# Kernel tuning notes

Hardware: AMD Instinct MI355X
Metric: run time of the kernel (lower is better)

The kernel has to match this reference:

```python
import jax, jax.numpy as jnp
import numpy as np

NUM_HEADS = 12


def setup_inputs() -> dict:
    key = jax.random.key(0)
    k1, k2, k3, k4, k5 = jax.random.split(key, 5)
    B, H, W, C = 8, 32, 32, 768
    x = jax.random.normal(k1, (B, H, W, C), dtype=jnp.float32)
    # torch nn.Linear weights: (out_features, in_features)
    qkv_w = jax.random.normal(k2, (3 * C, C), dtype=jnp.float32) * (C ** -0.5)
    qkv_b = jax.random.normal(k3, (3 * C,), dtype=jnp.float32) * 0.02
    proj_w = jax.random.normal(k4, (C, C), dtype=jnp.float32) * (C ** -0.5)
    proj_b = jax.random.normal(k5, (C,), dtype=jnp.float32) * 0.02
    return {"x": x, "qkv_w": qkv_w, "qkv_b": qkv_b, "proj_w": proj_w, "proj_b": proj_b}


def reference(x, qkv_w, qkv_b, proj_w, proj_b):
    B, H, W, C = x.shape
    nh = NUM_HEADS
    hd = C // nh
    scale = hd ** -0.5
    L = H * W
    # qkv projection: (B, L, 3C)
    qkv = jnp.einsum('bhwc,oc->bhwo', x, qkv_w) + qkv_b
    # -> (3, B*nh, L, hd)
    qkv = qkv.reshape(B, L, 3, nh, hd).transpose(2, 0, 3, 1, 4).reshape(3, B * nh, L, hd)
    q, k, v = qkv[0], qkv[1], qkv[2]
    # attention scores (B*nh, L, L)
    attn = jnp.einsum('bqd,bkd->bqk', q * scale, k)
    attn = jax.nn.softmax(attn, axis=-1)
    out = jnp.einsum('bqk,bkd->bqd', attn, v)  # (B*nh, L, hd)
    out = out.reshape(B, nh, H, W, hd).transpose(0, 2, 3, 1, 4).reshape(B, H, W, C)
    out = jnp.einsum('bhwc,oc->bhwo', out, proj_w) + proj_b
    return out
```

## Files before the change

### kernel.cpp

```cpp
#include <hip/hip_runtime.h>


typedef __attribute__((ext_vector_type(8))) __bf16 bf16x8;
typedef __attribute__((ext_vector_type(4))) __bf16 bf16x4;
typedef __attribute__((ext_vector_type(4))) float f32x4;

#define GLL16(g, l) __builtin_amdgcn_global_load_lds( \
    (const __attribute__((address_space(1))) void*)(g), \
    (__attribute__((address_space(3))) void*)(l), 16, 0, 0)

static __device__ __forceinline__ f32x4 mfma16(bf16x8 a, bf16x8 b, f32x4 c) {
  return __builtin_amdgcn_mfma_f32_16x16x32_bf16(a, b, c, 0, 0, 0);
}

static __device__ __forceinline__ float exp2_hw(float x) {
  return __builtin_amdgcn_exp2f(x);
}

static __device__ __forceinline__ int swz64(int row, int col) {
  return (row * 64 + col) ^ ((row & 7) << 3);
}

__global__ __launch_bounds__(256) void cvt_all(const float* __restrict__ x,
                                               const float* __restrict__ wq,
                                               const float* __restrict__ wp,
                                               __bf16* __restrict__ dst,
                                               int nx4, int nwq4, int total4) {
  const int i = blockIdx.x * 256 + threadIdx.x;
  if (i >= total4) return;
  const float* src;
  int off;
  if (i < nx4) { src = x; off = i; }
  else if (i < nx4 + nwq4) { src = wq; off = i - nx4; }
  else { src = wp; off = i - nx4 - nwq4; }
  const float4 v = *(const float4*)&src[(size_t)off * 4];
  bf16x4 o;
  o[0] = (__bf16)v.x; o[1] = (__bf16)v.y; o[2] = (__bf16)v.z; o[3] = (__bf16)v.w;
  *(bf16x4*)&dst[(size_t)i * 4] = o;
}

template <int EPI>
__global__ __launch_bounds__(256, 4) void gemm_nt(const __bf16* __restrict__ A,
                                                  const __bf16* __restrict__ Bw,
                                                  const float* __restrict__ bias,
                                                  float* __restrict__ out,
                                                  __bf16* __restrict__ Qb,
                                                  __bf16* __restrict__ Kb,
                                                  __bf16* __restrict__ Vtb,
                                                  int M, int N, int K) {
  __shared__ alignas(16) __bf16 smem[17408];
  const int tid = threadIdx.x;
  const int lane = tid & 63;
  const int wave = tid >> 6;
  const int wr = wave >> 1, wc = wave & 1;
  const int l15 = lane & 15, lhi = lane >> 4;
  const int mbase = blockIdx.x * 128;
  const int nbase = blockIdx.y * 128;

  f32x4 acc[4][4];
#pragma unroll
  for (int m = 0; m < 4; ++m)
#pragma unroll
    for (int n = 0; n < 4; ++n) acc[m][n] = (f32x4){0.f, 0.f, 0.f, 0.f};

  const int e0 = wave * 512 + lane * 8;
  const int e1 = e0 + 2048;
  const int ar0 = mbase + (e0 >> 5), ac0 = e0 & 31;
  const int ar1 = mbase + (e1 >> 5), ac1 = e1 & 31;
  const int br0 = nbase + (e0 >> 5);
  const int br1 = nbase + (e1 >> 5);

  const int nkt = K >> 5;

#define STAGE(t, bf) do { \
    const int kb_ = (t) << 5; \
    GLL16(A + (size_t)ar0 * K + kb_ + ac0, &smem[(bf) * 4096 + e0]); \
    GLL16(A + (size_t)ar1 * K + kb_ + ac1, &smem[(bf) * 4096 + e1]); \
    GLL16(Bw + (size_t)br0 * K + kb_ + ac0, &smem[8192 + (bf) * 4096 + e0]); \
    GLL16(Bw + (size_t)br1 * K + kb_ + ac1, &smem[8192 + (bf) * 4096 + e1]); \
  } while (0)

  STAGE(0, 0);

  for (int kt = 0; kt < nkt; ++kt) {
    const int cur = kt & 1;
    asm volatile("s_waitcnt vmcnt(0)" ::: "memory");
    __builtin_amdgcn_s_barrier();
    asm volatile("" ::: "memory");
    if (kt + 1 < nkt) STAGE(kt + 1, cur ^ 1);

    const __bf16* bufA = &smem[cur * 4096];
    const __bf16* bufB = &smem[8192 + cur * 4096];
    bf16x8 a[4], b[4];
#pragma unroll
    for (int m = 0; m < 4; ++m)
      a[m] = *(const bf16x8*)&bufA[(wr * 64 + m * 16 + l15) * 32 + lhi * 8];
#pragma unroll
    for (int n = 0; n < 4; ++n)
      b[n] = *(const bf16x8*)&bufB[(wc * 64 + n * 16 + l15) * 32 + lhi * 8];
#pragma unroll
    for (int m = 0; m < 4; ++m)
#pragma unroll
      for (int n = 0; n < 4; ++n)
        acc[m][n] = mfma16(a[m], b[n], acc[m][n]);
  }
#undef STAGE

  if (EPI == 0 && nbase >= 1536) {
    __syncthreads();
    __bf16* ldsT = &smem[0];
#pragma unroll
    for (int n = 0; n < 4; ++n) {
      const int gl = wc * 64 + n * 16 + l15;
      const float bv = bias[nbase + gl];
#pragma unroll
      for (int m = 0; m < 4; ++m) {
        bf16x4 pk;
#pragma unroll
        for (int i = 0; i < 4; ++i) pk[i] = (__bf16)(acc[m][n][i] + bv);
        *(bf16x4*)&ldsT[gl * 136 + wr * 64 + m * 16 + lhi * 4] = pk;
      }
    }
    __syncthreads();
    const int r = tid >> 1;
    const int half = tid & 1;
    const int head = ((nbase - 1536) >> 6) + (r >> 6);
    const int d = r & 63;
    const int bb = mbase >> 10;
    const int lbase = mbase & 1023;
    __bf16* dst = Vtb + ((size_t)(bb * 12 + head) * 64 + d) * 1024 + lbase + half * 64;
    const __bf16* srcl = &ldsT[r * 136 + half * 64];
#pragma unroll
    for (int j = 0; j < 8; ++j)
      *(bf16x8*)&dst[j * 8] = *(const bf16x8*)&srcl[j * 8];
    return;
  }

#pragma unroll
  for (int n = 0; n < 4; ++n) {
    const int gcol = nbase + wc * 64 + n * 16 + l15;
    const float bv = bias[gcol];
    if (EPI == 1) {
#pragma unroll
      for (int m = 0; m < 4; ++m)
#pragma unroll
        for (int i = 0; i < 4; ++i) {
          const int grow = mbase + wr * 64 + m * 16 + lhi * 4 + i;
          out[(size_t)grow * N + gcol] = acc[m][n][i] + bv;
        }
    } else {
      const int three = gcol / 768;
      const int rem = gcol - three * 768;
      const int head = rem >> 6;
      const int d = rem & 63;
#pragma unroll
      for (int m = 0; m < 4; ++m)
#pragma unroll
        for (int i = 0; i < 4; ++i) {
          const int grow = mbase + wr * 64 + m * 16 + lhi * 4 + i;
          const int bb = grow >> 10;
          const int lrow = grow & 1023;
          const int bh = bb * 12 + head;
          const float v = acc[m][n][i] + bv;
          if (three == 0)
            Qb[((size_t)bh * 1024 + lrow) * 64 + d] = (__bf16)(v * 0.18033688f);
          else
            Kb[((size_t)bh * 1024 + lrow) * 64 + d] = (__bf16)v;
        }
    }
  }
}

__global__ __launch_bounds__(512, 6) void attn_fwd(const __bf16* __restrict__ Q,
                                                   const __bf16* __restrict__ Kg,
                                                   const __bf16* __restrict__ Vt,
                                                   __bf16* __restrict__ O) {
  __shared__ alignas(16) __bf16 lK[2][64 * 64];
  __shared__ alignas(16) __bf16 lV[2][64 * 64];
  __shared__ alignas(16) __bf16 lP[8][16 * 72];
  const int tid = threadIdx.x, lane = tid & 63, wave = tid >> 6;
  const int l15 = lane & 15, lhi = lane >> 4;
  const int bh = blockIdx.x, qt = blockIdx.y;
  const int b = bh / 12, head = bh % 12;

  bf16x8 q[2];
  {
    const int qrow = qt * 128 + wave * 16 + l15;
#pragma unroll
    for (int kk = 0; kk < 2; ++kk)
      q[kk] = *(const bf16x8*)&Q[((size_t)bh * 1024 + qrow) * 64 + kk * 32 + lhi * 8];
  }

  f32x4 o[4];
  float mrun = -3.0e38f, lrun = 0.f;
#pragma unroll
  for (int n = 0; n < 4; ++n) o[n] = (f32x4){0.f, 0.f, 0.f, 0.f};

  const int q0b = tid * 16;
  const int p0b = q0b ^ (((q0b >> 7) & 7) << 4);
  const int e0 = q0b >> 1;
  const int kofs0 = p0b >> 1;
  const int vofs0 = (p0b >> 7) * 1024 + ((p0b & 127) >> 1);

  const __bf16* kbase = Kg + (size_t)bh * 1024 * 64;
  const __bf16* vbase = Vt + (size_t)bh * 64 * 1024;

  GLL16(kbase + kofs0, &lK[0][e0]);
  GLL16(vbase + vofs0, &lV[0][e0]);
  __syncthreads();

  for (int kv = 0; kv < 16; ++kv) {
    const int cur = kv & 1;
    if (kv + 1 < 16) {
      GLL16(kbase + (kv + 1) * 4096 + kofs0, &lK[cur ^ 1][e0]);
      GLL16(vbase + (kv + 1) * 64 + vofs0, &lV[cur ^ 1][e0]);
    }

    f32x4 s[4];
#pragma unroll
    for (int km = 0; km < 4; ++km) {
      bf16x8 k0 = *(const bf16x8*)&lK[cur][swz64(km * 16 + l15, lhi * 8)];
      bf16x8 k1 = *(const bf16x8*)&lK[cur][swz64(km * 16 + l15, 32 + lhi * 8)];
      f32x4 z = (f32x4){0.f, 0.f, 0.f, 0.f};
      z = mfma16(k0, q[0], z);
      z = mfma16(k1, q[1], z);
      s[km] = z;
    }

    float lm = s[0][0];
#pragma unroll
    for (int km = 0; km < 4; ++km)
#pragma unroll
      for (int i = 0; i < 4; ++i) lm = fmaxf(lm, s[km][i]);

    if (!__all(lm - mrun <= 8.f)) {
      float r = lm;
      r = fmaxf(r, __shfl_xor(r, 16));
      r = fmaxf(r, __shfl_xor(r, 32));
      const float mnew = fmaxf(mrun, r);
      const float alpha = exp2_hw(mrun - mnew);
      mrun = mnew;
      lrun *= alpha;
      float am[4];
#pragma unroll
      for (int i = 0; i < 4; ++i) am[i] = __shfl(alpha, (lhi << 2) | i, 64);
#pragma unroll
      for (int n = 0; n < 4; ++n)
#pragma unroll
        for (int i = 0; i < 4; ++i) o[n][i] *= am[i];
    }

    {
      float ps = 0.f;
#pragma unroll
      for (int km = 0; km < 4; ++km) {
        bf16x4 pk;
#pragma unroll
        for (int i = 0; i < 4; ++i) {
          const float p = exp2_hw(s[km][i] - mrun);
          ps += p;
          pk[i] = (__bf16)p;
        }
        *(bf16x4*)&lP[wave][l15 * 72 + km * 16 + lhi * 4] = pk;
      }
      lrun += ps;
    }

    bf16x8 vf[4][2];
#pragma unroll
    for (int n = 0; n < 4; ++n)
#pragma unroll
      for (int kk = 0; kk < 2; ++kk)
        vf[n][kk] = *(const bf16x8*)&lV[cur][swz64(n * 16 + l15, kk * 32 + lhi * 8)];
    {
      bf16x8 p0 = *(const bf16x8*)&lP[wave][l15 * 72 + lhi * 8];
      bf16x8 p1 = *(const bf16x8*)&lP[wave][l15 * 72 + 32 + lhi * 8];
#pragma unroll
      for (int n = 0; n < 4; ++n) {
        o[n] = mfma16(p0, vf[n][0], o[n]);
        o[n] = mfma16(p1, vf[n][1], o[n]);
      }
    }
    __syncthreads();
  }

  float r = lrun;
  r += __shfl_xor(r, 16);
  r += __shfl_xor(r, 32);
  const float inv = 1.f / r;
  float im[4];
#pragma unroll
  for (int i = 0; i < 4; ++i) im[i] = __shfl(inv, (lhi << 2) | i, 64);
#pragma unroll
  for (int i = 0; i < 4; ++i) {
    const int lrow = qt * 128 + wave * 16 + lhi * 4 + i;
#pragma unroll
    for (int n = 0; n < 4; ++n) {
      const int col = head * 64 + n * 16 + l15;
      O[((size_t)b * 1024 + lrow) * 768 + col] = (__bf16)(o[n][i] * im[i]);
    }
  }
}

extern "C" void kernel_launch(void* const* d_in, const int* in_sizes, int n_in,
                              void* d_out, int out_size, void* d_ws, size_t ws_size,
                              hipStream_t stream) {
  const float* x = (const float*)d_in[0];
  const float* qkv_w = (const float*)d_in[1];
  const float* qkv_b = (const float*)d_in[2];
  const float* proj_w = (const float*)d_in[3];
  const float* proj_b = (const float*)d_in[4];
  float* out = (float*)d_out;

  const size_t NX = (size_t)8192 * 768;
  const size_t NWQ = (size_t)2304 * 768;
  const size_t NWP = (size_t)768 * 768;
  const size_t SZ = (size_t)96 * 1024 * 64;

  __bf16* xb = (__bf16*)d_ws;
  __bf16* wqkvb = xb + NX;
  __bf16* wprojb = wqkvb + NWQ;
  __bf16* Q = wprojb + NWP;
  __bf16* K = Q + SZ;
  __bf16* Vt = K + SZ;
  __bf16* AO = Vt + SZ;

  const int nx4 = (int)(NX / 4), nwq4 = (int)(NWQ / 4), nwp4 = (int)(NWP / 4);
  const int total4 = nx4 + nwq4 + nwp4;
  cvt_all<<<(total4 + 255) / 256, 256, 0, stream>>>(x, qkv_w, proj_w, xb, nx4, nwq4, total4);

  gemm_nt<0><<<dim3(64, 18), 256, 0, stream>>>(xb, wqkvb, qkv_b, nullptr, Q, K, Vt,
                                               8192, 2304, 768);
  attn_fwd<<<dim3(96, 8), 512, 0, stream>>>(Q, K, Vt, AO);
  gemm_nt<1><<<dim3(64, 6), 256, 0, stream>>>(AO, wprojb, proj_b, out,
                                              nullptr, nullptr, nullptr, 8192, 768, 768);
}
```

Baseline: 115.7 us.

## Double GEMM K-tile to 64 with XOR-swizzled LDS layout

The bf16 NT GEMM now stages K-tiles of 64 instead of 32. This halves the number of barrier/wait iterations and doubles the MFMA work per sync. The LDS layout is XOR-swizzled: global loads gather pre-swizzled source addresses so that the row-stride-64 fragment reads avoid bank conflicts. LDS use per block roughly doubles to 64KB, and launch bounds drop to 2 blocks per CU, which reduces occupancy.

```diff
diff --git a/kernel.cpp b/kernel.cpp
--- a/kernel.cpp
+++ b/kernel.cpp
@@ -19,6 +19,9 @@
 
 static __device__ __forceinline__ int swz64(int row, int col) {
   return (row * 64 + col) ^ ((row & 7) << 3);
+}
+static __device__ __forceinline__ int swz64e(int e) {
+  return e ^ (((e >> 6) & 7) << 3);
 }
 
 __global__ __launch_bounds__(256) void cvt_all(const float* __restrict__ x,
@@ -40,7 +43,7 @@
 }
 
 template <int EPI>
-__global__ __launch_bounds__(256, 4) void gemm_nt(const __bf16* __restrict__ A,
+__global__ __launch_bounds__(256, 2) void gemm_nt(const __bf16* __restrict__ A,
                                                   const __bf16* __restrict__ Bw,
                                                   const float* __restrict__ bias,
                                                   float* __restrict__ out,
@@ -48,7 +51,7 @@
                                                   __bf16* __restrict__ Kb,
                                                   __bf16* __restrict__ Vtb,
                                                   int M, int N, int K) {
-  __shared__ alignas(16) __bf16 smem[17408];
+  __shared__ alignas(16) __bf16 smem[32768];
   const int tid = threadIdx.x;
   const int lane = tid & 63;
   const int wave = tid >> 6;
@@ -63,21 +66,28 @@
 #pragma unroll
     for (int n = 0; n < 4; ++n) acc[m][n] = (f32x4){0.f, 0.f, 0.f, 0.f};
 
-  const int e0 = wave * 512 + lane * 8;
-  const int e1 = e0 + 2048;
-  const int ar0 = mbase + (e0 >> 5), ac0 = e0 & 31;
-  const int ar1 = mbase + (e1 >> 5), ac1 = e1 & 31;
-  const int br0 = nbase + (e0 >> 5);
-  const int br1 = nbase + (e1 >> 5);
-
-  const int nkt = K >> 5;
+  int srow[4], scol[4];
+#pragma unroll
+  for (int c = 0; c < 4; ++c) {
+    const int e = c * 2048 + tid * 8;
+    const int se = swz64e(e);
+    srow[c] = se >> 6;
+    scol[c] = se & 63;
+  }
+  const int eD = tid * 8;
+
+  const int nkt = K >> 6;
 
 #define STAGE(t, bf) do { \
-    const int kb_ = (t) << 5; \
-    GLL16(A + (size_t)ar0 * K + kb_ + ac0, &smem[(bf) * 4096 + e0]); \
-    GLL16(A + (size_t)ar1 * K + kb_ + ac1, &smem[(bf) * 4096 + e1]); \
-    GLL16(Bw + (size_t)br0 * K + kb_ + ac0, &smem[8192 + (bf) * 4096 + e0]); \
-    GLL16(Bw + (size_t)br1 * K + kb_ + ac1, &smem[8192 + (bf) * 4096 + e1]); \
+    const int kb_ = (t) << 6; \
+    GLL16(A + (size_t)(mbase + srow[0]) * K + kb_ + scol[0], &smem[(bf) * 8192 + 0 * 2048 + eD]); \
+    GLL16(A + (size_t)(mbase + srow[1]) * K + kb_ + scol[1], &smem[(bf) * 8192 + 1 * 2048 + eD]); \
+    GLL16(A + (size_t)(mbase + srow[2]) * K + kb_ + scol[2], &smem[(bf) * 8192 + 2 * 2048 + eD]); \
+    GLL16(A + (size_t)(mbase + srow[3]) * K + kb_ + scol[3], &smem[(bf) * 8192 + 3 * 2048 + eD]); \
+    GLL16(Bw + (size_t)(nbase + srow[0]) * K + kb_ + scol[0], &smem[16384 + (bf) * 8192 + 0 * 2048 + eD]); \
+    GLL16(Bw + (size_t)(nbase + srow[1]) * K + kb_ + scol[1], &smem[16384 + (bf) * 8192 + 1 * 2048 + eD]); \
+    GLL16(Bw + (size_t)(nbase + srow[2]) * K + kb_ + scol[2], &smem[16384 + (bf) * 8192 + 2 * 2048 + eD]); \
+    GLL16(Bw + (size_t)(nbase + srow[3]) * K + kb_ + scol[3], &smem[16384 + (bf) * 8192 + 3 * 2048 + eD]); \
   } while (0)
 
   STAGE(0, 0);
@@ -89,20 +99,23 @@
     asm volatile("" ::: "memory");
     if (kt + 1 < nkt) STAGE(kt + 1, cur ^ 1);
 
-    const __bf16* bufA = &smem[cur * 4096];
-    const __bf16* bufB = &smem[8192 + cur * 4096];
-    bf16x8 a[4], b[4];
-#pragma unroll
-    for (int m = 0; m < 4; ++m)
-      a[m] = *(const bf16x8*)&bufA[(wr * 64 + m * 16 + l15) * 32 + lhi * 8];
-#pragma unroll
-    for (int n = 0; n < 4; ++n)
-      b[n] = *(const bf16x8*)&bufB[(wc * 64 + n * 16 + l15) * 32 + lhi * 8];
-#pragma unroll
-    for (int m = 0; m < 4; ++m)
+    const __bf16* bufA = &smem[cur * 8192];
+    const __bf16* bufB = &smem[16384 + cur * 8192];
+#pragma unroll
+    for (int kk = 0; kk < 2; ++kk) {
+      bf16x8 a[4], b[4];
+#pragma unroll
+      for (int m = 0; m < 4; ++m)
+        a[m] = *(const bf16x8*)&bufA[swz64(wr * 64 + m * 16 + l15, kk * 32 + lhi * 8)];
 #pragma unroll
       for (int n = 0; n < 4; ++n)
-        acc[m][n] = mfma16(a[m], b[n], acc[m][n]);
+        b[n] = *(const bf16x8*)&bufB[swz64(wc * 64 + n * 16 + l15, kk * 32 + lhi * 8)];
+#pragma unroll
+      for (int m = 0; m < 4; ++m)
+#pragma unroll
+        for (int n = 0; n < 4; ++n)
+          acc[m][n] = mfma16(a[m], b[n], acc[m][n]);
+    }
   }
 #undef STAGE
 
```

Result: faster. 107.9 us (-6.7%).
